# Kernel tuning notes

Hardware: AMD Instinct MI355X
Metric: run time of the kernel (lower is better)

Reference implementation:

```python
import jax, jax.numpy as jnp
import numpy as np

B, C, H, Wd = 16, 256, 64, 64
D_MODEL = 256


def setup_inputs() -> dict:
    key = jax.random.key(0)
    kx, kw = jax.random.split(key)
    x = jax.random.normal(kx, (B, C, H, Wd), dtype=jnp.float32)
    # 1x1 conv weight [out_c=1+2*d_model, in_c], scaled like kaiming-ish init
    W = jax.random.normal(kw, (1 + 2 * D_MODEL, C), dtype=jnp.float32) / np.sqrt(C)
    return {"x": x, "W": W}


def reference(x, W):
    b, c, h, w = x.shape
    d = (W.shape[0] - 1) // 2
    n = h * w
    xf = x.reshape(b, c, n)                      # [b, c, N]
    qkv = jnp.einsum('oc,bcn->bon', W, xf)       # 1x1 conv == channel GEMM
    q = qkv[:, :1]                               # [b, 1, N]
    k = qkv[:, 1:1 + d]                          # [b, d, N]
    v = qkv[:, 1 + d:]                           # [b, d, N]
    scores = jax.nn.softmax(q, axis=-1)          # softmax over tokens
    ctx = jnp.sum(k * scores, axis=-1, keepdims=True)  # [b, d, 1]
    out = jax.nn.relu(v) * ctx                   # gated ReLU(v)
    return out.reshape(b, d, h, w)
```

## Files before the change

### kernel.cpp

```cpp
#include <hip/hip_runtime.h>
#include <cstdint>
#include <cstddef>

#define NB 16
#define NC 256
#define NN 4096
#define ND 256

typedef unsigned short u16;
typedef unsigned int u32;

typedef __attribute__((ext_vector_type(8))) short short8;
typedef __attribute__((ext_vector_type(4))) float f32x4;

__device__ __forceinline__ u16 f2bf(float f) {
  union { float f; u32 u; } v; v.f = f;
  u32 r = v.u + 0x7FFFu + ((v.u >> 16) & 1u);
  return (u16)(r >> 16);
}
__device__ __forceinline__ float bf2f(u16 h) {
  union { u32 u; float f; } v; v.u = ((u32)h) << 16; return v.f;
}

__global__ __launch_bounds__(256) void k_fuse1(const float* __restrict__ x,
                                               const float* __restrict__ W,
                                               u16* __restrict__ xbT,
                                               u16* __restrict__ wvb,
                                               float* __restrict__ pm,
                                               float* __restrict__ pl,
                                               float* __restrict__ pacc) {
  __shared__ float qred[32 * 65];
  __shared__ float qred2[4 * 65];
  const int t = threadIdx.x;
  const int b = blockIdx.y, n0 = blockIdx.x * 64;
  const int tx = t & 7, ty = t >> 3;
  const int c0 = ty * 8, nl = tx * 8;
  const float* xb = x + (size_t)b * NC * NN + n0;

  const float4 w0 = *(const float4*)(W + c0);
  const float4 w1 = *(const float4*)(W + c0 + 4);
  const float wq[8] = {w0.x, w0.y, w0.z, w0.w, w1.x, w1.y, w1.z, w1.w};

  short8 pk[8];
  float qp[8] = {0.f, 0.f, 0.f, 0.f, 0.f, 0.f, 0.f, 0.f};

#pragma unroll
  for (int r = 0; r < 8; ++r) {
    const float* xr = xb + (size_t)(c0 + r) * NN + nl;
    const float4 va = *(const float4*)(xr);
    const float4 vb = *(const float4*)(xr + 4);
    qp[0] += wq[r] * va.x; qp[1] += wq[r] * va.y;
    qp[2] += wq[r] * va.z; qp[3] += wq[r] * va.w;
    qp[4] += wq[r] * vb.x; qp[5] += wq[r] * vb.y;
    qp[6] += wq[r] * vb.z; qp[7] += wq[r] * vb.w;
    pk[0][r] = (short)f2bf(va.x); pk[1][r] = (short)f2bf(va.y);
    pk[2][r] = (short)f2bf(va.z); pk[3][r] = (short)f2bf(va.w);
    pk[4][r] = (short)f2bf(vb.x); pk[5][r] = (short)f2bf(vb.y);
    pk[6][r] = (short)f2bf(vb.z); pk[7][r] = (short)f2bf(vb.w);
  }

  u16* ob = xbT + (size_t)(b * NN + n0 + nl) * NC + c0;
#pragma unroll
  for (int j = 0; j < 8; ++j)
    *(short8*)(ob + (size_t)j * NC) = pk[j];

#pragma unroll
  for (int j = 0; j < 8; ++j) qred[ty * 65 + nl + j] = qp[j];
  __syncthreads();
  {
    const int n = t & 63, g = t >> 6;
    float s = 0.f;
#pragma unroll
    for (int k = 0; k < 8; ++k) s += qred[(g * 8 + k) * 65 + n];
    qred2[g * 65 + n] = s;
  }
  __syncthreads();

  float q[8];
#pragma unroll
  for (int j = 0; j < 8; ++j)
    q[j] = qred2[0 * 65 + nl + j] + qred2[1 * 65 + nl + j] +
           qred2[2 * 65 + nl + j] + qred2[3 * 65 + nl + j];

  float m = q[0];
#pragma unroll
  for (int j = 1; j < 8; ++j) m = fmaxf(m, q[j]);
#pragma unroll
  for (int off = 1; off < 8; off <<= 1) m = fmaxf(m, __shfl_xor(m, off));

  float p[8]; float l = 0.f;
#pragma unroll
  for (int j = 0; j < 8; ++j) { p[j] = __expf(q[j] - m); l += p[j]; }
#pragma unroll
  for (int off = 1; off < 8; off <<= 1) l += __shfl_xor(l, off);

  float sc[8];
#pragma unroll
  for (int r = 0; r < 8; ++r) {
    float s = 0.f;
#pragma unroll
    for (int j = 0; j < 8; ++j) s += bf2f((u16)pk[j][r]) * p[j];
    sc[r] = s;
  }
#pragma unroll
  for (int off = 1; off < 8; off <<= 1) {
#pragma unroll
    for (int r = 0; r < 8; ++r) sc[r] += __shfl_xor(sc[r], off);
  }
  if (tx == 0) {
    float* pp = pacc + ((size_t)b * 64 + blockIdx.x) * NC + c0;
#pragma unroll
    for (int r = 0; r < 8; ++r) pp[r] = sc[r];
  }
  if (t == 0) {
    pm[b * 64 + blockIdx.x] = m;
    pl[b * 64 + blockIdx.x] = l;
  }

  if (b == 0 && blockIdx.x < 8) {
    const float* wv = W + (size_t)(1 + ND) * NC;
    const int base = blockIdx.x * 8192;
#pragma unroll
    for (int i = 0; i < 8; ++i) {
      const int idx = base + i * 1024 + t * 4;
      const float4 v = *(const float4*)(wv + idx);
      ushort4 o = {f2bf(v.x), f2bf(v.y), f2bf(v.z), f2bf(v.w)};
      *(ushort4*)(wvb + idx) = o;
    }
  }
}

#define BM 256
#define BN 128
#define BK 64

__global__ __launch_bounds__(512) void k_gemm(const u16* __restrict__ xbT,
                                              const u16* __restrict__ wvb,
                                              const float* __restrict__ W,
                                              const float* __restrict__ pm,
                                              const float* __restrict__ pl,
                                              const float* __restrict__ pacc,
                                              float* __restrict__ out) {
  __shared__ __align__(16) u16 As[BM * BK];
  __shared__ __align__(16) u16 Bs[BN * BK];
  __shared__ float am[64], al[64];
  __shared__ __align__(16) float sx[NC];
  __shared__ float sctx[NC];

  const int t = threadIdx.x;
  const int b = blockIdx.y;
  const int n0 = blockIdx.x * BN;
  const int lane = t & 63, w = t >> 6;
  const int wd = (w >> 1) * 64, wn = (w & 1) * 64;
  const int quad = lane >> 4, l15 = lane & 15;

  const int rstg = t >> 3;
  const int l8 = ((t & 7) ^ (rstg & 7)) * 8;
  const u16* gA = wvb + (size_t)rstg * NC + l8;
  const u16* gB = xbT + (size_t)(b * NN + n0 + rstg) * NC + l8;
  const int ldst = 8 * t;

#pragma unroll
  for (int i = 0; i < 4; ++i)
    __builtin_amdgcn_global_load_lds(
        (const __attribute__((address_space(1))) u32*)(gA + (size_t)(64 * i) * NC),
        (__attribute__((address_space(3))) u32*)(As + 4096 * i + ldst), 16, 0, 0);
#pragma unroll
  for (int i = 0; i < 2; ++i)
    __builtin_amdgcn_global_load_lds(
        (const __attribute__((address_space(1))) u32*)(gB + (size_t)(64 * i) * NC),
        (__attribute__((address_space(3))) u32*)(Bs + 4096 * i + ldst), 16, 0, 0);

  if (t < 64) { am[t] = pm[b * 64 + t]; al[t] = pl[b * 64 + t]; }
  __syncthreads();

  float M2 = -3.4e38f;
#pragma unroll
  for (int i = 0; i < 64; ++i) M2 = fmaxf(M2, am[i]);
  if (t < 256) {
    float xsv = 0.f, L2s = 0.f;
#pragma unroll 8
    for (int i = 0; i < 64; ++i) {
      const float wgt = __expf(am[i] - M2);
      L2s += wgt * al[i];
      xsv += wgt * pacc[(size_t)(b * 64 + i) * NC + t];
    }
    sx[t] = xsv / L2s;
  }
  __syncthreads();
  if (t < 256) {
    const float* wk = W + (size_t)(1 + t) * NC;
    float a = 0.f;
#pragma unroll 4
    for (int c4 = 0; c4 < 64; ++c4) {
      const float4 w4 = *(const float4*)(wk + c4 * 4);
      const float4 s4 = *(const float4*)&sx[c4 * 4];
      a += w4.x * s4.x + w4.y * s4.y + w4.z * s4.z + w4.w * s4.w;
    }
    sctx[t] = a;
  }

  f32x4 acc[4][4];
#pragma unroll
  for (int ni = 0; ni < 4; ++ni)
#pragma unroll
    for (int mi = 0; mi < 4; ++mi)
      acc[ni][mi] = (f32x4){0.f, 0.f, 0.f, 0.f};

  const int pq0 = ((0 * 4 + quad) ^ (l15 & 7)) * 8;
  const int pq1 = ((1 * 4 + quad) ^ (l15 & 7)) * 8;

  for (int kk = 0; kk < NC; kk += BK) {
    if (kk) {
      __syncthreads();
#pragma unroll
      for (int i = 0; i < 4; ++i)
        __builtin_amdgcn_global_load_lds(
            (const __attribute__((address_space(1))) u32*)(gA + kk + (size_t)(64 * i) * NC),
            (__attribute__((address_space(3))) u32*)(As + 4096 * i + ldst), 16, 0, 0);
#pragma unroll
      for (int i = 0; i < 2; ++i)
        __builtin_amdgcn_global_load_lds(
            (const __attribute__((address_space(1))) u32*)(gB + kk + (size_t)(64 * i) * NC),
            (__attribute__((address_space(3))) u32*)(Bs + 4096 * i + ldst), 16, 0, 0);
      __syncthreads();
    }

#pragma unroll
    for (int kq = 0; kq < 2; ++kq) {
      const int pq = kq ? pq1 : pq0;
      short8 xf[4], wf[4];
#pragma unroll
      for (int ni = 0; ni < 4; ++ni)
        xf[ni] = *(const short8*)&Bs[(wn + ni * 16 + l15) * BK + pq];
#pragma unroll
      for (int mi = 0; mi < 4; ++mi)
        wf[mi] = *(const short8*)&As[(wd + mi * 16 + l15) * BK + pq];
#pragma unroll
      for (int ni = 0; ni < 4; ++ni)
#pragma unroll
        for (int mi = 0; mi < 4; ++mi)
          acc[ni][mi] = __builtin_amdgcn_mfma_f32_16x16x32_bf16(xf[ni], wf[mi],
                                                                acc[ni][mi], 0, 0, 0);
    }
  }

#pragma unroll
  for (int mi = 0; mi < 4; ++mi) {
    const int d = wd + mi * 16 + l15;
    const float cx = sctx[d];
    float* op = out + (size_t)(b * NC + d) * NN + n0 + wn + quad * 4;
#pragma unroll
    for (int ni = 0; ni < 4; ++ni) {
      f32x4 v = acc[ni][mi];
      v[0] = fmaxf(v[0], 0.f) * cx;
      v[1] = fmaxf(v[1], 0.f) * cx;
      v[2] = fmaxf(v[2], 0.f) * cx;
      v[3] = fmaxf(v[3], 0.f) * cx;
      __builtin_nontemporal_store(v, (f32x4*)(op + ni * 16));
    }
  }
}

extern "C" void kernel_launch(void* const* d_in, const int* in_sizes, int n_in,
                              void* d_out, int out_size, void* d_ws, size_t ws_size,
                              hipStream_t stream) {
  const float* x = (const float*)d_in[0];
  const float* W = (const float*)d_in[1];
  float* out = (float*)d_out;

  char* ws = (char*)d_ws;
  u16* xbT    = (u16*)ws;
  float* pacc = (float*)(ws + 33554432);
  float* pm   = (float*)(ws + 34603008);
  float* pl   = (float*)(ws + 34607104);
  u16* wvb    = (u16*)(ws + 34611200);

  k_fuse1<<<dim3(64, 16), 256, 0, stream>>>(x, W, xbT, wvb, pm, pl, pacc);
  k_gemm<<<dim3(32, 16), 512, 0, stream>>>(xbT, wvb, W, pm, pl, pacc, out);
}
```

Measured before the change: 154.0 us.

## Load GEMM fragments directly from global memory instead of LDS staging

Removes the LDS tiles and the global_load_lds staging with its per-K-step barriers, so each wave loads its bf16 MFMA fragments straight from global memory (relying on L1/L2 for reuse). This frees LDS and drops the synchronization inside the K loop, and lets the compiler schedule loads across the fully unrolled K loop. The cost is redundant global/cache traffic, since each A and B row is now fetched separately by multiple waves. The prologue loads no longer overlap with the ctx computation, and a barrier is added after sctx is written.

```diff
diff --git a/kernel.cpp b/kernel.cpp
--- a/kernel.cpp
+++ b/kernel.cpp
@@ -130,9 +130,7 @@
   }
 }
 
-#define BM 256
 #define BN 128
-#define BK 64
 
 __global__ __launch_bounds__(512) void k_gemm(const u16* __restrict__ xbT,
                                               const u16* __restrict__ wvb,
@@ -141,8 +139,6 @@
                                               const float* __restrict__ pl,
                                               const float* __restrict__ pacc,
                                               float* __restrict__ out) {
-  __shared__ __align__(16) u16 As[BM * BK];
-  __shared__ __align__(16) u16 Bs[BN * BK];
   __shared__ float am[64], al[64];
   __shared__ __align__(16) float sx[NC];
   __shared__ float sctx[NC];
@@ -154,26 +150,8 @@
   const int wd = (w >> 1) * 64, wn = (w & 1) * 64;
   const int quad = lane >> 4, l15 = lane & 15;
 
-  const int rstg = t >> 3;
-  const int l8 = ((t & 7) ^ (rstg & 7)) * 8;
-  const u16* gA = wvb + (size_t)rstg * NC + l8;
-  const u16* gB = xbT + (size_t)(b * NN + n0 + rstg) * NC + l8;
-  const int ldst = 8 * t;
-
-#pragma unroll
-  for (int i = 0; i < 4; ++i)
-    __builtin_amdgcn_global_load_lds(
-        (const __attribute__((address_space(1))) u32*)(gA + (size_t)(64 * i) * NC),
-        (__attribute__((address_space(3))) u32*)(As + 4096 * i + ldst), 16, 0, 0);
-#pragma unroll
-  for (int i = 0; i < 2; ++i)
-    __builtin_amdgcn_global_load_lds(
-        (const __attribute__((address_space(1))) u32*)(gB + (size_t)(64 * i) * NC),
-        (__attribute__((address_space(3))) u32*)(Bs + 4096 * i + ldst), 16, 0, 0);
-
   if (t < 64) { am[t] = pm[b * 64 + t]; al[t] = pl[b * 64 + t]; }
   __syncthreads();
-
   float M2 = -3.4e38f;
 #pragma unroll
   for (int i = 0; i < 64; ++i) M2 = fmaxf(M2, am[i]);
@@ -199,6 +177,7 @@
     }
     sctx[t] = a;
   }
+  __syncthreads();
 
   f32x4 acc[4][4];
 #pragma unroll
@@ -207,42 +186,24 @@
     for (int mi = 0; mi < 4; ++mi)
       acc[ni][mi] = (f32x4){0.f, 0.f, 0.f, 0.f};
 
-  const int pq0 = ((0 * 4 + quad) ^ (l15 & 7)) * 8;
-  const int pq1 = ((1 * 4 + quad) ^ (l15 & 7)) * 8;
-
-  for (int kk = 0; kk < NC; kk += BK) {
-    if (kk) {
-      __syncthreads();
-#pragma unroll
-      for (int i = 0; i < 4; ++i)
-        __builtin_amdgcn_global_load_lds(
-            (const __attribute__((address_space(1))) u32*)(gA + kk + (size_t)(64 * i) * NC),
-            (__attribute__((address_space(3))) u32*)(As + 4096 * i + ldst), 16, 0, 0);
-#pragma unroll
-      for (int i = 0; i < 2; ++i)
-        __builtin_amdgcn_global_load_lds(
-            (const __attribute__((address_space(1))) u32*)(gB + kk + (size_t)(64 * i) * NC),
-            (__attribute__((address_space(3))) u32*)(Bs + 4096 * i + ldst), 16, 0, 0);
-      __syncthreads();
-    }
-
-#pragma unroll
-    for (int kq = 0; kq < 2; ++kq) {
-      const int pq = kq ? pq1 : pq0;
-      short8 xf[4], wf[4];
-#pragma unroll
-      for (int ni = 0; ni < 4; ++ni)
-        xf[ni] = *(const short8*)&Bs[(wn + ni * 16 + l15) * BK + pq];
+  const u16* pA = wvb + (size_t)(wd + l15) * NC + quad * 8;
+  const u16* pB = xbT + (size_t)(b * NN + n0 + wn + l15) * NC + quad * 8;
+
+#pragma unroll
+  for (int kc = 0; kc < 8; ++kc) {
+    short8 xf[4], wf[4];
+#pragma unroll
+    for (int ni = 0; ni < 4; ++ni)
+      xf[ni] = *(const short8*)(pB + (size_t)(ni * 16) * NC + kc * 32);
+#pragma unroll
+    for (int mi = 0; mi < 4; ++mi)
+      wf[mi] = *(const short8*)(pA + (size_t)(mi * 16) * NC + kc * 32);
+#pragma unroll
+    for (int ni = 0; ni < 4; ++ni)
 #pragma unroll
       for (int mi = 0; mi < 4; ++mi)
-        wf[mi] = *(const short8*)&As[(wd + mi * 16 + l15) * BK + pq];
-#pragma unroll
-      for (int ni = 0; ni < 4; ++ni)
-#pragma unroll
-        for (int mi = 0; mi < 4; ++mi)
-          acc[ni][mi] = __builtin_amdgcn_mfma_f32_16x16x32_bf16(xf[ni], wf[mi],
-                                                                acc[ni][mi], 0, 0, 0);
-    }
+        acc[ni][mi] = __builtin_amdgcn_mfma_f32_16x16x32_bf16(xf[ni], wf[mi],
+                                                              acc[ni][mi], 0, 0, 0);
   }
 
 #pragma unroll
```

Result: slower. 177.3 us (+15.1%).
